# Kernel optimization log

Hardware: AMD Instinct MI355X
Metric: run time of the kernel (lower is better)

## Reference

```python
import jax, jax.numpy as jnp
import numpy as np

D = 384      # d_model
H = 12       # num_heads
DK = 32      # head dim
L = 6        # num_layers
FF = 1536    # FFN intermediate (4*d_model)
EPS = 1e-12  # BERT LayerNorm eps


def layer_norm(x, w, b):
    m = jnp.mean(x, -1, keepdims=True)
    v = jnp.mean((x - m) ** 2, -1, keepdims=True)
    return (x - m) * jax.lax.rsqrt(v + EPS) * w + b


def deltanet(x, mask, Wq, bq, Wk, bk, Wv, bv, Wb, bb, Wg, bg, Wo, bo, fl, sl):
    # Hierarchical delta-rule linear attention with fast/slow decay states.
    B, S, _ = x.shape
    q = (x @ Wq + bq).reshape(B, S, H, DK)
    k = (x @ Wk + bk).reshape(B, S, H, DK)
    k = k / (jnp.linalg.norm(k, axis=-1, keepdims=True) + 1e-6)
    v = (x @ Wv + bv).reshape(B, S, H, DK)
    beta = jax.nn.sigmoid(x @ Wb + bb) * mask[:, :, None]   # [B,S,H] write gate
    g = jax.nn.sigmoid(x @ Wg + bg)                          # [B,S,H] flux mix gate
    af = jax.nn.sigmoid(fl)[None, :, None, None]             # fast decay, init 0.3
    as_ = jax.nn.sigmoid(sl)[None, :, None, None]            # slow decay, init 0.85

    def step(carry, inp):
        Sf, Ss = carry                      # [B,H,DK,DK] states
        qt, kt, vt, bt, gt = inp            # [B,H,DK],[B,H,DK],[B,H,DK],[B,H],[B,H]
        rf = jnp.einsum('bhkd,bhk->bhd', Sf, kt)
        Sf = af * Sf + bt[..., None, None] * kt[..., :, None] * (vt - rf)[:, :, None, :]
        of = jnp.einsum('bhkd,bhk->bhd', Sf, qt)
        rs = jnp.einsum('bhkd,bhk->bhd', Ss, kt)
        Ss = as_ * Ss + bt[..., None, None] * kt[..., :, None] * (vt - rs)[:, :, None, :]
        os_ = jnp.einsum('bhkd,bhk->bhd', Ss, qt)
        out = gt[..., None] * of + (1.0 - gt[..., None]) * os_
        return (Sf, Ss), out

    to_t = lambda a: jnp.moveaxis(a, 1, 0)  # [B,S,...] -> [S,B,...]
    S0 = jnp.zeros((B, H, DK, DK), x.dtype)
    _, out = jax.lax.scan(step, (S0, S0), (to_t(q), to_t(k), to_t(v), to_t(beta), to_t(g)))
    out = jnp.moveaxis(out, 0, 1).reshape(B, S, D)
    return out @ Wo + bo


def _forward(input_ids, attention_mask, word_emb, pos_emb, type_emb, emb_ln_w, emb_ln_b,
             Wq, bq, Wk, bk, Wv, bv, Wbeta, bbeta, Wg, bg, Wo, bo, fast_logit, slow_logit,
             attn_ln_w, attn_ln_b, ffn_w1, ffn_b1, ffn_w2, ffn_b2, ffn_ln_w, ffn_ln_b):
    B, S = input_ids.shape
    mask = attention_mask.astype(jnp.float32)
    x = word_emb[input_ids] + pos_emb[:S][None] + type_emb[0][None, None]
    x = layer_norm(x, emb_ln_w, emb_ln_b)
    for i in range(L):
        res = x
        a = deltanet(x, mask, Wq[i], bq[i], Wk[i], bk[i], Wv[i], bv[i],
                     Wbeta[i], bbeta[i], Wg[i], bg[i], Wo[i], bo[i],
                     fast_logit[i], slow_logit[i])
        x = layer_norm(res + a, attn_ln_w[i], attn_ln_b[i])
        res = x
        h = jax.nn.gelu(x @ ffn_w1[i] + ffn_b1[i], approximate=False)
        x = layer_norm(res + h @ ffn_w2[i] + ffn_b2[i], ffn_ln_w[i], ffn_ln_b[i])
    m = mask[:, :, None]
    emb = jnp.sum(x * m, 1) / jnp.clip(jnp.sum(m, 1), 1e-9)
    return emb / jnp.linalg.norm(emb, axis=1, keepdims=True)


def setup_inputs() -> dict:
    key = jax.random.key(0)
    ks = jax.random.split(key, 16)
    B, S, V, P = 64, 512, 30522, 512
    n = lambda k, shp, s=0.02: jax.random.normal(k, shp, jnp.float32) * s
    return {
        'input_ids': jax.random.randint(ks[0], (B, S), 0, V),
        'attention_mask': jnp.ones((B, S), jnp.int32),
        'word_emb': n(ks[1], (V, D)),
        'pos_emb': n(ks[2], (P, D)),
        'type_emb': n(ks[3], (2, D)),
        'emb_ln_w': jnp.ones((D,)), 'emb_ln_b': jnp.zeros((D,)),
        'Wq': n(ks[4], (L, D, D)), 'bq': jnp.zeros((L, D)),
        'Wk': n(ks[5], (L, D, D)), 'bk': jnp.zeros((L, D)),
        'Wv': n(ks[6], (L, D, D)), 'bv': jnp.zeros((L, D)),
        'Wbeta': n(ks[7], (L, D, H)), 'bbeta': jnp.zeros((L, H)),
        'Wg': n(ks[8], (L, D, H)), 'bg': jnp.zeros((L, H)),
        'Wo': n(ks[9], (L, D, D)), 'bo': jnp.zeros((L, D)),
        'fast_logit': jnp.full((L, H), -0.8473, jnp.float32),  # sigmoid -> 0.3
        'slow_logit': jnp.full((L, H), 1.7346, jnp.float32),   # sigmoid -> 0.85
        'attn_ln_w': jnp.ones((L, D)), 'attn_ln_b': jnp.zeros((L, D)),
        'ffn_w1': n(ks[10], (L, D, FF)), 'ffn_b1': jnp.zeros((L, FF)),
        'ffn_w2': n(ks[11], (L, FF, D)), 'ffn_b2': jnp.zeros((L, D)),
        'ffn_ln_w': jnp.ones((L, D)), 'ffn_ln_b': jnp.zeros((L, D)),
    }


def reference(input_ids, attention_mask, word_emb, pos_emb, type_emb, emb_ln_w, emb_ln_b,
              Wq, bq, Wk, bk, Wv, bv, Wbeta, bbeta, Wg, bg, Wo, bo, fast_logit, slow_logit,
              attn_ln_w, attn_ln_b, ffn_w1, ffn_b1, ffn_w2, ffn_b2, ffn_ln_w, ffn_ln_b):
    return _forward(input_ids, attention_mask, word_emb, pos_emb, type_emb, emb_ln_w, emb_ln_b,
                    Wq, bq, Wk, bk, Wv, bv, Wbeta, bbeta, Wg, bg, Wo, bo, fast_logit, slow_logit,
                    attn_ln_w, attn_ln_b, ffn_w1, ffn_b1, ffn_w2, ffn_b2, ffn_ln_w, ffn_ln_b)
```

## Files before the change

kernel.cpp:

```cpp
#include <hip/hip_runtime.h>
#include <math.h>

#define DD 384
#define HH 12
#define DKK 32
#define LL 6
#define FFF 1536
#define BB 64
#define SS 512
#define MROWS (BB*SS)
#define TB 32
#define LDX 1152

typedef _Float16 f16;
typedef _Float16 half8 __attribute__((ext_vector_type(8)));
typedef _Float16 h2 __attribute__((ext_vector_type(2)));
typedef float f32x4 __attribute__((ext_vector_type(4)));
typedef float f32x2 __attribute__((ext_vector_type(2)));

__device__ __forceinline__ float sigmoidf_(float x){ return 1.0f/(1.0f+expf(-x)); }

__device__ __forceinline__ float h2f_lo(unsigned int u){
  union { unsigned short s; f16 h; } c; c.s = (unsigned short)(u & 0xffffu); return (float)c.h;
}
__device__ __forceinline__ float h2f_hi(unsigned int u){
  union { unsigned short s; f16 h; } c; c.s = (unsigned short)(u >> 16); return (float)c.h;
}

__device__ __forceinline__ void gl2lds16(const void* g, void* l){
  __builtin_amdgcn_global_load_lds((const __attribute__((address_space(1))) void*)g,
                                   (__attribute__((address_space(3))) void*)l, 16, 0, 0);
}

__global__ __launch_bounds__(256) void embed_ln_kernel(
    const int* __restrict__ ids, const float* __restrict__ we,
    const float* __restrict__ pe, const float* __restrict__ te,
    const float* __restrict__ w, const float* __restrict__ b,
    float* __restrict__ x, f16* __restrict__ xh)
{
  int wv = threadIdx.x >> 6, lane = threadIdx.x & 63;
  int row = blockIdx.x * 4 + wv;
  int s = row & (SS-1);
  int id = ids[row];
  const float* wep = we + (size_t)id * DD;
  const float* pep = pe + (size_t)s * DD;
  float vals[6]; float sum = 0.f;
  #pragma unroll
  for (int i=0;i<6;i++){ int d = lane + 64*i; vals[i] = wep[d] + pep[d] + te[d]; sum += vals[i]; }
  #pragma unroll
  for (int off=32; off>=1; off>>=1) sum += __shfl_xor(sum, off);
  float mean = sum * (1.0f/DD);
  float vs = 0.f;
  #pragma unroll
  for (int i=0;i<6;i++){ float dv = vals[i]-mean; vs += dv*dv; }
  #pragma unroll
  for (int off=32; off>=1; off>>=1) vs += __shfl_xor(vs, off);
  float inv = rsqrtf(vs*(1.0f/DD) + 1e-12f);
  float* xr = x + (size_t)row*DD;
  f16* xhr = xh + (size_t)row*DD;
  #pragma unroll
  for (int i=0;i<6;i++){ int d = lane + 64*i; float o = (vals[i]-mean)*inv*w[d] + b[d]; xr[d]=o; xhr[d]=(f16)o; }
}

template<int YH>
__global__ __launch_bounds__(256) void add_ln_kernel(
    float* __restrict__ x, f16* __restrict__ xh, const void* __restrict__ yp,
    const float* __restrict__ w, const float* __restrict__ b, int row0, int ldy)
{
  int wv = threadIdx.x >> 6, lane = threadIdx.x & 63;
  int rrel = blockIdx.x * 4 + wv;
  int row = row0 + rrel;
  float* xr = x + (size_t)row*DD;
  f16* xhr = xh + (size_t)row*DD;
  float vals[6]; float sum = 0.f;
  #pragma unroll
  for (int i=0;i<6;i++){
    int d = lane + 64*i;
    float yv;
    if (YH) yv = (float)((const f16*)yp)[(size_t)rrel*ldy + d];
    else    yv = ((const float*)yp)[(size_t)rrel*ldy + d];
    vals[i] = xr[d] + yv; sum += vals[i];
  }
  #pragma unroll
  for (int off=32; off>=1; off>>=1) sum += __shfl_xor(sum, off);
  float mean = sum * (1.0f/DD);
  float vs = 0.f;
  #pragma unroll
  for (int i=0;i<6;i++){ float dv = vals[i]-mean; vs += dv*dv; }
  #pragma unroll
  for (int off=32; off>=1; off>>=1) vs += __shfl_xor(vs, off);
  float inv = rsqrtf(vs*(1.0f/DD) + 1e-12f);
  #pragma unroll
  for (int i=0;i<6;i++){ int d = lane + 64*i; float o = (vals[i]-mean)*inv*w[d] + b[d]; xr[d]=o; xhr[d]=(f16)o; }
}

__global__ __launch_bounds__(256) void biaspack_kernel(
    const float* __restrict__ bq, const float* __restrict__ bk, const float* __restrict__ bv,
    float* __restrict__ dst)
{
  int i = blockIdx.x*256 + threadIdx.x;
  if (i >= LL*LDX) return;
  int l = i / LDX, r = i - l*LDX;
  float v;
  if (r < 384) v = bq[l*DD + r];
  else if (r < 768) v = bk[l*DD + r-384];
  else v = bv[l*DD + r-768];
  dst[i] = v;
}

__global__ __launch_bounds__(256) void wtrans_kernel(
  const float* __restrict__ Wq, const float* __restrict__ Wk, const float* __restrict__ Wv,
  const float* __restrict__ Wo, const float* __restrict__ W1, const float* __restrict__ W2,
  f16* __restrict__ Wt)
{
  __shared__ float T[32][33];
  int l = blockIdx.x / 1728, bidx = blockIdx.x % 1728;
  const float* src; f16* dst; int K, N, tile;
  if (bidx < 576){ int m = bidx/144; tile = bidx - m*144; K=384; N=384;
    const float* w4[4] = {Wq + (size_t)l*147456, Wk + (size_t)l*147456,
                          Wv + (size_t)l*147456, Wo + (size_t)l*147456};
    src = w4[m]; dst = Wt + (size_t)l*1769472 + m*147456; }
  else if (bidx < 1152){ tile = bidx-576; K=384; N=1536;
    src = W1 + (size_t)l*589824; dst = Wt + (size_t)l*1769472 + 589824; }
  else { tile = bidx-1152; K=1536; N=384;
    src = W2 + (size_t)l*589824; dst = Wt + (size_t)l*1769472 + 1179648; }
  int tN = N>>5;
  int tk = tile / tN, tn = tile - tk*tN;
  int k0 = tk<<5, n0 = tn<<5;
  int r = threadIdx.x >> 3, c4 = (threadIdx.x & 7) << 2;
  float4 vv = *(const float4*)(src + (size_t)(k0+r)*N + n0 + c4);
  T[r][c4+0]=vv.x; T[r][c4+1]=vv.y; T[r][c4+2]=vv.z; T[r][c4+3]=vv.w;
  __syncthreads();
  f16* dp = dst + (size_t)(n0+r)*K + k0 + c4;
  #pragma unroll
  for (int j=0;j<4;j++) dp[j] = (f16)T[c4+j][r];
}

template<int ACT, int OUT16>
__global__ __launch_bounds__(256) void gemm_f16(
    const f16* __restrict__ A, const f16* __restrict__ BT,
    const float* __restrict__ bias, float* __restrict__ Cf, f16* __restrict__ Ch,
    int M, int N, int K, int lda, int ldc)
{
  __shared__ __align__(16) f16 As0[128*32];
  __shared__ __align__(16) f16 As1[128*32];
  __shared__ __align__(16) f16 Bs0[128*32];
  __shared__ __align__(16) f16 Bs1[128*32];
  int tid = threadIdx.x, lane = tid & 63, wave = tid >> 6;
  int wm = wave >> 1, wn = wave & 1;
  int n0 = blockIdx.x * 128, m0 = blockIdx.y * 128;
  f32x4 acc[4][4] = {};
  int seg0 = wave*2048 + lane*16;
  int ar = lane & 15, kq = (lane >> 4) * 8;

  for (int k0=0; k0<K; k0+=64){
    #pragma unroll
    for (int i=0;i<2;i++){
      int seg = seg0 + i*1024;
      int e = seg >> 1; int row = e >> 5; int kk = e & 31;
      const f16* ap = A  + (size_t)(m0+row)*lda + k0 + kk;
      const f16* bp = BT + (size_t)(n0+row)*K   + k0 + kk;
      gl2lds16(ap,      (char*)As0 + seg);
      gl2lds16(ap + 32, (char*)As1 + seg);
      gl2lds16(bp,      (char*)Bs0 + seg);
      gl2lds16(bp + 32, (char*)Bs1 + seg);
    }
    __syncthreads();
    {
      half8 af[4], bf[4];
      #pragma unroll
      for (int mi=0;mi<4;mi++) af[mi] = *(const half8*)&As0[(wm*64 + mi*16 + ar)*32 + kq];
      #pragma unroll
      for (int ni=0;ni<4;ni++) bf[ni] = *(const half8*)&Bs0[(wn*64 + ni*16 + ar)*32 + kq];
      #pragma unroll
      for (int mi=0;mi<4;mi++)
        #pragma unroll
        for (int ni=0;ni<4;ni++)
          acc[mi][ni] = __builtin_amdgcn_mfma_f32_16x16x32_f16(af[mi], bf[ni], acc[mi][ni], 0, 0, 0);
    }
    {
      half8 af[4], bf[4];
      #pragma unroll
      for (int mi=0;mi<4;mi++) af[mi] = *(const half8*)&As1[(wm*64 + mi*16 + ar)*32 + kq];
      #pragma unroll
      for (int ni=0;ni<4;ni++) bf[ni] = *(const half8*)&Bs1[(wn*64 + ni*16 + ar)*32 + kq];
      #pragma unroll
      for (int mi=0;mi<4;mi++)
        #pragma unroll
        for (int ni=0;ni<4;ni++)
          acc[mi][ni] = __builtin_amdgcn_mfma_f32_16x16x32_f16(af[mi], bf[ni], acc[mi][ni], 0, 0, 0);
    }
    __syncthreads();
  }
  int rb = (lane >> 4) * 4, cb = lane & 15;
  #pragma unroll
  for (int ni=0;ni<4;ni++){
    int cn = n0 + wn*64 + ni*16 + cb;
    float bz = bias[cn];
    #pragma unroll
    for (int mi=0;mi<4;mi++){
      int rm = m0 + wm*64 + mi*16 + rb;
      #pragma unroll
      for (int r=0;r<4;r++){
        float v = acc[mi][ni][r] + bz;
        if (ACT==1) v = 0.5f*v*(1.0f+erff(v*0.70710678118f));
        if (OUT16) Ch[(size_t)(rm+r)*ldc + cn] = (f16)v;
        else       Cf[(size_t)(rm+r)*ldc + cn] = v;
      }
    }
  }
}

__global__ __launch_bounds__(256) void betag_kernel(
    const float* __restrict__ x, const float* __restrict__ Wb, const float* __restrict__ bb,
    const float* __restrict__ Wg, const float* __restrict__ bg,
    const int* __restrict__ mask, float* __restrict__ beta, float* __restrict__ g)
{
  __shared__ float Ws[384*25];
  for (int idx = threadIdx.x; idx < 384*12; idx += 256){
    int k = idx/12, j = idx - k*12;
    Ws[k*25+j]    = Wb[idx];
    Ws[k*25+12+j] = Wg[idx];
  }
  __syncthreads();
  int wv = threadIdx.x>>6, lane = threadIdx.x&63;
  int row = blockIdx.x*4 + wv;
  const float* xr = x + (size_t)row*DD;
  float accb[12], accg[12];
  #pragma unroll
  for (int j=0;j<12;j++){ accb[j]=0.f; accg[j]=0.f; }
  #pragma unroll
  for (int i=0;i<6;i++){
    int k = lane + 64*i;
    float xv = xr[k];
    const float* wr = &Ws[k*25];
    #pragma unroll
    for (int j=0;j<12;j++){ accb[j] += xv*wr[j]; accg[j] += xv*wr[12+j]; }
  }
  #pragma unroll
  for (int j=0;j<12;j++){
    #pragma unroll
    for (int off=32; off>=1; off>>=1){
      accb[j]+=__shfl_xor(accb[j],off);
      accg[j]+=__shfl_xor(accg[j],off);
    }
  }
  if (lane==0){
    float mk = (float)mask[row];
    #pragma unroll
    for (int j=0;j<12;j++){
      beta[(size_t)row*HH + j] = sigmoidf_(accb[j]+bb[j]) * mk;
      g[(size_t)row*HH + j]    = sigmoidf_(accg[j]+bg[j]);
    }
  }
}

__global__ __launch_bounds__(64) void scan_kernel(
  f16* qkv,
  const float* __restrict__ bp, const float* __restrict__ gp,
  const float* __restrict__ flp, const float* __restrict__ slp)
{
  __shared__ float Kf[2][TB][32];
  __shared__ float Qf[2][TB][32];
  __shared__ float Vf[2][TB][32];
  __shared__ float Bg[2][2][TB];
  __shared__ float Of[TB][64];
  int blk = blockIdx.x;
  int b = blk / HH, h = blk - b*HH;
  int lane = threadIdx.x;
  int col = lane & 31;
  float a = sigmoidf_((lane < 32) ? flp[h] : slp[h]);
  f32x2 a2 = {a, a};
  f32x2 S2[16];
  #pragma unroll
  for (int j=0;j<16;j++) S2[j] = (f32x2){0.f,0.f};
  size_t base = ((size_t)b*SS)*LDX + (size_t)h*DKK;
  f16* qb = qkv + base;
  const f16* kb = qkv + base + 384;
  const f16* vb = qkv + base + 768;
  const float* bbp = bp + ((size_t)b*SS)*HH + h;
  const float* gbp = gp + ((size_t)b*SS)*HH + h;

  int st0 = lane >> 2, part = lane & 3;
  uint4 kv[2], qv[2], vv[2]; float bgv;

  #define LOADG(T0) do {                                                       \
    _Pragma("unroll")                                                          \
    for (int r=0;r<2;r++){                                                     \
      int st = (T0) + r*16 + st0;                                              \
      size_t off = (size_t)st*LDX + part*8;                                    \
      kv[r] = *(const uint4*)(kb + off);                                       \
      qv[r] = *(const uint4*)(qb + off);                                       \
      vv[r] = *(const uint4*)(vb + off);                                       \
    }                                                                          \
    int tb_ = (T0) + (lane & 31);                                              \
    bgv = (lane < 32) ? bbp[(size_t)tb_*HH] : gbp[(size_t)tb_*HH];             \
  } while(0)

  #define STAGE(BUF) do {                                                      \
    _Pragma("unroll")                                                          \
    for (int r=0;r<2;r++){                                                     \
      int s = r*16 + st0;                                                      \
      float kf[8], qf[8], vf[8];                                               \
      kf[0]=h2f_lo(kv[r].x); kf[1]=h2f_hi(kv[r].x); kf[2]=h2f_lo(kv[r].y);     \
      kf[3]=h2f_hi(kv[r].y); kf[4]=h2f_lo(kv[r].z); kf[5]=h2f_hi(kv[r].z);     \
      kf[6]=h2f_lo(kv[r].w); kf[7]=h2f_hi(kv[r].w);                            \
      qf[0]=h2f_lo(qv[r].x); qf[1]=h2f_hi(qv[r].x); qf[2]=h2f_lo(qv[r].y);     \
      qf[3]=h2f_hi(qv[r].y); qf[4]=h2f_lo(qv[r].z); qf[5]=h2f_hi(qv[r].z);     \
      qf[6]=h2f_lo(qv[r].w); qf[7]=h2f_hi(qv[r].w);                            \
      vf[0]=h2f_lo(vv[r].x); vf[1]=h2f_hi(vv[r].x); vf[2]=h2f_lo(vv[r].y);     \
      vf[3]=h2f_hi(vv[r].y); vf[4]=h2f_lo(vv[r].z); vf[5]=h2f_hi(vv[r].z);     \
      vf[6]=h2f_lo(vv[r].w); vf[7]=h2f_hi(vv[r].w);                            \
      float ss = 0.f;                                                          \
      _Pragma("unroll")                                                        \
      for (int i=0;i<8;i++) ss += kf[i]*kf[i];                                 \
      ss += __shfl_xor(ss, 1); ss += __shfl_xor(ss, 2);                        \
      float sc = 1.0f/(sqrtf(ss)+1e-6f);                                       \
      float4 t;                                                                \
      t.x=kf[0]*sc; t.y=kf[1]*sc; t.z=kf[2]*sc; t.w=kf[3]*sc;                  \
      *(float4*)&Kf[BUF][s][part*8] = t;                                       \
      t.x=kf[4]*sc; t.y=kf[5]*sc; t.z=kf[6]*sc; t.w=kf[7]*sc;                  \
      *(float4*)&Kf[BUF][s][part*8+4] = t;                                     \
      t.x=qf[0]; t.y=qf[1]; t.z=qf[2]; t.w=qf[3];                              \
      *(float4*)&Qf[BUF][s][part*8] = t;                                       \
      t.x=qf[4]; t.y=qf[5]; t.z=qf[6]; t.w=qf[7];                              \
      *(float4*)&Qf[BUF][s][part*8+4] = t;                                     \
      t.x=vf[0]; t.y=vf[1]; t.z=vf[2]; t.w=vf[3];                              \
      *(float4*)&Vf[BUF][s][part*8] = t;                                       \
      t.x=vf[4]; t.y=vf[5]; t.z=vf[6]; t.w=vf[7];                              \
      *(float4*)&Vf[BUF][s][part*8+4] = t;                                     \
    }                                                                          \
    Bg[BUF][lane>>5][lane&31] = bgv;                                           \
  } while(0)

  #define LDSTEP(BUF,S,KR,QR,VT,BT) do {                                       \
    const float4* k4_ = (const float4*)&Kf[BUF][S][0];                         \
    const float4* q4_ = (const float4*)&Qf[BUF][S][0];                         \
    _Pragma("unroll")                                                          \
    for (int j=0;j<8;j++){ KR[j]=k4_[j]; QR[j]=q4_[j]; }                       \
    VT = Vf[BUF][S][col]; BT = Bg[BUF][0][S];                                  \
  } while(0)

  #define STEP(KR,QR,VT,BT,S) do {                                            \
    const f32x2* k2_ = (const f32x2*)KR;                                       \
    const f32x2* q2_ = (const f32x2*)QR;                                       \
    f32x2 rA={0.f,0.f},rB={0.f,0.f},rC={0.f,0.f},rD={0.f,0.f};                 \
    _Pragma("unroll")                                                          \
    for (int j=0;j<16;j+=4){                                                   \
      rA += S2[j+0]*k2_[j+0]; rB += S2[j+1]*k2_[j+1];                          \
      rC += S2[j+2]*k2_[j+2]; rD += S2[j+3]*k2_[j+3]; }                        \
    f32x2 rr = (rA+rB)+(rC+rD);                                                \
    float rf = rr.x + rr.y;                                                    \
    float c_ = (BT)*((VT) - rf);                                               \
    f32x2 c2 = {c_, c_};                                                       \
    _Pragma("unroll")                                                          \
    for (int j=0;j<16;j++) S2[j] = a2*S2[j] + c2*k2_[j];                       \
    f32x2 oA={0.f,0.f},oB={0.f,0.f},oC={0.f,0.f},oD={0.f,0.f};                 \
    _Pragma("unroll")                                                          \
    for (int j=0;j<16;j+=4){                                                   \
      oA += S2[j+0]*q2_[j+0]; oB += S2[j+1]*q2_[j+1];                          \
      oC += S2[j+2]*q2_[j+2]; oD += S2[j+3]*q2_[j+3]; }                        \
    f32x2 oo = (oA+oB)+(oC+oD);                                                \
    Of[S][lane] = oo.x + oo.y;                                                 \
  } while(0)

  #define COMBINE(BUF,T0) do {                                                 \
    _Pragma("unroll")                                                          \
    for (int i=0;i<16;i++){                                                    \
      int idx = i*64 + lane;                                                   \
      int s_ = idx >> 5, c_ = idx & 31;                                        \
      float fv = Of[s_][c_];                                                   \
      float sv = Of[s_][c_+32];                                                \
      float gv = Bg[BUF][1][s_];                                               \
      qb[(size_t)((T0)+s_)*LDX + c_] = (f16)(gv*fv + (1.0f-gv)*sv);            \
    }                                                                          \
  } while(0)

  LOADG(0);
  STAGE(0);
  __syncthreads();

  float4 kA[8], qA[8], kB[8], qB[8];
  float vA, bA, vB, bB;

  for (int tile=0; tile<SS/TB; tile++){
    int buf = tile & 1;
    if (tile < SS/TB-1) LOADG((tile+1)*TB);
    LDSTEP(buf, 0, kA, qA, vA, bA);
    #pragma unroll
    for (int s=0; s<TB; s+=2){
      if (s+1 < TB) LDSTEP(buf, s+1, kB, qB, vB, bB);
      STEP(kA, qA, vA, bA, s);
      if (s+2 < TB) LDSTEP(buf, s+2, kA, qA, vA, bA);
      STEP(kB, qB, vB, bB, s+1);
    }
    if (tile < SS/TB-1) STAGE(1-buf);
    COMBINE(buf, tile*TB);
    __syncthreads();
  }
  #undef LOADG
  #undef STAGE
  #undef LDSTEP
  #undef STEP
  #undef COMBINE
}

__global__ __launch_bounds__(384) void pool_kernel(
    const float* __restrict__ x, const int* __restrict__ mask, float* __restrict__ out)
{
  __shared__ float red[384];
  __shared__ float tot;
  int b = blockIdx.x, d = threadIdx.x;
  const float* xb = x + (size_t)b*SS*DD;
  const int* mb = mask + b*SS;
  float s=0.f, sm=0.f;
  for (int t=0;t<SS;t++){ float m=(float)mb[t]; s += xb[(size_t)t*DD+d]*m; sm += m; }
  float emb = s / fmaxf(sm, 1e-9f);
  red[d] = emb*emb;
  __syncthreads();
  for (int off=192; off>=3; off>>=1){
    if (d < off) red[d] += red[d+off];
    __syncthreads();
  }
  if (d==0) tot = red[0]+red[1]+red[2];
  __syncthreads();
  out[(size_t)b*DD + d] = emb * rsqrtf(tot);
}

extern "C" void kernel_launch(void* const* d_in, const int* in_sizes, int n_in,
                              void* d_out, int out_size, void* d_ws, size_t ws_size,
                              hipStream_t stream)
{
  const int*   ids  = (const int*)d_in[0];
  const int*   amask= (const int*)d_in[1];
  const float* we   = (const float*)d_in[2];
  const float* pe   = (const float*)d_in[3];
  const float* te   = (const float*)d_in[4];
  const float* elnw = (const float*)d_in[5];
  const float* elnb = (const float*)d_in[6];
  const float* Wq   = (const float*)d_in[7];
  const float* bq   = (const float*)d_in[8];
  const float* Wk   = (const float*)d_in[9];
  const float* bk   = (const float*)d_in[10];
  const float* Wv   = (const float*)d_in[11];
  const float* bv   = (const float*)d_in[12];
  const float* Wb   = (const float*)d_in[13];
  const float* bb   = (const float*)d_in[14];
  const float* Wg   = (const float*)d_in[15];
  const float* bgp  = (const float*)d_in[16];
  const float* Wo   = (const float*)d_in[17];
  const float* bo   = (const float*)d_in[18];
  const float* fl   = (const float*)d_in[19];
  const float* sl   = (const float*)d_in[20];
  const float* alnw = (const float*)d_in[21];
  const float* alnb = (const float*)d_in[22];
  const float* W1   = (const float*)d_in[23];
  const float* b1   = (const float*)d_in[24];
  const float* W2   = (const float*)d_in[25];
  const float* b2   = (const float*)d_in[26];
  const float* flnw = (const float*)d_in[27];
  const float* flnb = (const float*)d_in[28];
  float* out = (float*)d_out;
  float* w = (float*)d_ws;

  float* x    = w;
  f16*  xh   = (f16*)(w + 12582912);
  f16*  qkvh = (f16*)(w + 18874368);
  float* f2   = w + 37748736;
  float* beta = f2 + 3145728;
  float* gbuf = beta + 393216;
  f16*  wt   = (f16*)(w + 44040192);
  float* bqkv = w + 49348608;
  f16*  hb   = qkvh;

  embed_ln_kernel<<<MROWS/4, 256, 0, stream>>>(ids, we, pe, te, elnw, elnb, x, xh);
  biaspack_kernel<<<27,256,0,stream>>>(bq, bk, bv, bqkv);
  wtrans_kernel<<<LL*1728,256,0,stream>>>(Wq, Wk, Wv, Wo, W1, W2, wt);

  for (int l=0;l<LL;l++){
    f16* wl = wt + (size_t)l*1769472;

    gemm_f16<0,1><<<dim3(9,256),256,0,stream>>>(xh, wl, bqkv + l*LDX, nullptr, qkvh,
                                                MROWS, LDX, DD, DD, LDX);

    betag_kernel<<<MROWS/4,256,0,stream>>>(x, Wb + (size_t)l*DD*HH, bb + l*HH,
                                           Wg + (size_t)l*DD*HH, bgp + l*HH,
                                           amask, beta, gbuf);
    scan_kernel<<<BB*HH,64,0,stream>>>(qkvh, beta, gbuf, fl + l*HH, sl + l*HH);

    gemm_f16<0,1><<<dim3(3,256),256,0,stream>>>(qkvh, wl+442368, bo+l*DD, nullptr,
                                                qkvh + 384, MROWS, DD, DD, LDX, LDX);
    add_ln_kernel<1><<<MROWS/4,256,0,stream>>>(x, xh, qkvh + 384, alnw+l*DD, alnb+l*DD, 0, LDX);

    gemm_f16<1,1><<<dim3(12,256),256,0,stream>>>(xh, wl+589824, b1+l*FFF, nullptr, hb,
                                                 MROWS, FFF, DD, DD, FFF);
    gemm_f16<0,1><<<dim3(3,256),256,0,stream>>>(hb, wl+1179648, b2+l*DD, nullptr, xh,
                                                MROWS, DD, FFF, FFF, DD);
    add_ln_kernel<1><<<MROWS/4,256,0,stream>>>(x, xh, xh, flnw+l*DD, flnb+l*DD, 0, DD);
  }

  pool_kernel<<<BB,384,0,stream>>>(x, amask, out);
}
```

Before: 3.504 ms.

## Double-buffer GEMM LDS tiles and swizzle block order across XCDs

The GEMM kernel now prefetches the next K-tile into a second LDS buffer while computing on the current one. This removes the load-then-sync stall on every iteration. Block indices are also remapped so that consecutive hardware block IDs, which are dispatched round-robin across chiplets, get contiguous tile ranges for better L2 locality. LDS use doubles to 64KB per block, which can reduce occupancy, and the remap assumes the grid size is divisible by 8.

Result: faster. 3.373 ms (-3.7%).

```diff
diff --git a/kernel.cpp b/kernel.cpp
--- a/kernel.cpp
+++ b/kernel.cpp
@@ -142,56 +142,58 @@
     const float* __restrict__ bias, float* __restrict__ Cf, f16* __restrict__ Ch,
     int M, int N, int K, int lda, int ldc)
 {
-  __shared__ __align__(16) f16 As0[128*32];
-  __shared__ __align__(16) f16 As1[128*32];
-  __shared__ __align__(16) f16 Bs0[128*32];
-  __shared__ __align__(16) f16 Bs1[128*32];
+  __shared__ __align__(16) f16 As[2][2][128*32];
+  __shared__ __align__(16) f16 Bs[2][2][128*32];
   int tid = threadIdx.x, lane = tid & 63, wave = tid >> 6;
   int wm = wave >> 1, wn = wave & 1;
-  int n0 = blockIdx.x * 128, m0 = blockIdx.y * 128;
+  int gx = gridDim.x, gy = gridDim.y;
+  int bid = blockIdx.y * gx + blockIdx.x;
+  int chunk = (gx * gy) >> 3;
+  int nf = (bid & 7) * chunk + (bid >> 3);
+  int tx = nf / gy, ty = nf - tx * gy;
+  int n0 = tx * 128, m0 = ty * 128;
   f32x4 acc[4][4] = {};
   int seg0 = wave*2048 + lane*16;
   int ar = lane & 15, kq = (lane >> 4) * 8;
 
-  for (int k0=0; k0<K; k0+=64){
+  #define GSTAGE(PB, K0) do {                                                  \
+    _Pragma("unroll")                                                          \
+    for (int i=0;i<2;i++){                                                     \
+      int seg = seg0 + i*1024;                                                 \
+      int e = seg >> 1; int row = e >> 5; int kk = e & 31;                     \
+      const f16* ap = A  + (size_t)(m0+row)*lda + (K0) + kk;                   \
+      const f16* bp = BT + (size_t)(n0+row)*K   + (K0) + kk;                   \
+      gl2lds16(ap,      (char*)As[PB][0] + seg);                               \
+      gl2lds16(ap + 32, (char*)As[PB][1] + seg);                               \
+      gl2lds16(bp,      (char*)Bs[PB][0] + seg);                               \
+      gl2lds16(bp + 32, (char*)Bs[PB][1] + seg);                               \
+    }                                                                          \
+  } while(0)
+
+  GSTAGE(0, 0);
+  __syncthreads();
+  int nk = K >> 6;
+  int pb = 0;
+  for (int t=0; t<nk; t++){
+    if (t+1 < nk) GSTAGE(pb^1, (t+1)*64);
     #pragma unroll
-    for (int i=0;i<2;i++){
-      int seg = seg0 + i*1024;
-      int e = seg >> 1; int row = e >> 5; int kk = e & 31;
-      const f16* ap = A  + (size_t)(m0+row)*lda + k0 + kk;
-      const f16* bp = BT + (size_t)(n0+row)*K   + k0 + kk;
-      gl2lds16(ap,      (char*)As0 + seg);
-      gl2lds16(ap + 32, (char*)As1 + seg);
-      gl2lds16(bp,      (char*)Bs0 + seg);
-      gl2lds16(bp + 32, (char*)Bs1 + seg);
-    }
-    __syncthreads();
-    {
-      half8 af[4], bf[4];
+    for (int h=0; h<2; h++){
+      half8 af[4], bfr[4];
       #pragma unroll
-      for (int mi=0;mi<4;mi++) af[mi] = *(const half8*)&As0[(wm*64 + mi*16 + ar)*32 + kq];
+      for (int mi=0;mi<4;mi++) af[mi]  = *(const half8*)&As[pb][h][(wm*64 + mi*16 + ar)*32 + kq];
       #pragma unroll
-      for (int ni=0;ni<4;ni++) bf[ni] = *(const half8*)&Bs0[(wn*64 + ni*16 + ar)*32 + kq];
+      for (int ni=0;ni<4;ni++) bfr[ni] = *(const half8*)&Bs[pb][h][(wn*64 + ni*16 + ar)*32 + kq];
       #pragma unroll
       for (int mi=0;mi<4;mi++)
         #pragma unroll
         for (int ni=0;ni<4;ni++)
-          acc[mi][ni] = __builtin_amdgcn_mfma_f32_16x16x32_f16(af[mi], bf[ni], acc[mi][ni], 0, 0, 0);
-    }
-    {
-      half8 af[4], bf[4];
-      #pragma unroll
-      for (int mi=0;mi<4;mi++) af[mi] = *(const half8*)&As1[(wm*64 + mi*16 + ar)*32 + kq];
-      #pragma unroll
-      for (int ni=0;ni<4;ni++) bf[ni] = *(const half8*)&Bs1[(wn*64 + ni*16 + ar)*32 + kq];
-      #pragma unroll
-      for (int mi=0;mi<4;mi++)
-        #pragma unroll
-        for (int ni=0;ni<4;ni++)
-          acc[mi][ni] = __builtin_amdgcn_mfma_f32_16x16x32_f16(af[mi], bf[ni], acc[mi][ni], 0, 0, 0);
+          acc[mi][ni] = __builtin_amdgcn_mfma_f32_16x16x32_f16(af[mi], bfr[ni], acc[mi][ni], 0, 0, 0);
     }
     __syncthreads();
-  }
+    pb ^= 1;
+  }
+  #undef GSTAGE
+
   int rb = (lane >> 4) * 4, cb = lane & 15;
   #pragma unroll
   for (int ni=0;ni<4;ni++){
```
